# Kernel tuning notes

Measured on AMD Instinct MI355X. Metric: run time of the kernel, lower is better.

## Reference

```python
import jax, jax.numpy as jnp
import numpy as np

B, T, C = 2, 2048, 1024
H = 16
HD = C // H  # head_size = 64
FF = 2 * C   # ffwd_size default = n_embd * 2
EPS = float(jnp.finfo(jnp.float32).eps)  # torch RMSNorm eps=None -> finfo eps


def rmsnorm(x, g):
    # torch.nn.RMSNorm: x / sqrt(mean(x^2) + eps) * weight
    ms = jnp.mean(jnp.square(x), axis=-1, keepdims=True)
    return x * jax.lax.rsqrt(ms + EPS) * g


def setup_inputs() -> dict:
    key = jax.random.key(0)
    ks = jax.random.split(key, 12)
    s_in = 1.0 / np.sqrt(C)
    s_ff = 1.0 / np.sqrt(FF)
    return {
        "target": jax.random.normal(ks[0], (B, T, C), dtype=jnp.float32),
        # per-head projections, torch Linear layout [out, in] stacked over heads: [H, HD, C]
        "wq": jax.random.uniform(ks[1], (H, HD, C), jnp.float32, -s_in, s_in),
        "wk": jax.random.uniform(ks[2], (H, HD, C), jnp.float32, -s_in, s_in),
        "wv": jax.random.uniform(ks[3], (H, HD, C), jnp.float32, -s_in, s_in),
        "w_proj": jax.random.uniform(ks[4], (C, H * HD), jnp.float32, -s_in, s_in),
        "b_proj": jax.random.uniform(ks[5], (C,), jnp.float32, -s_in, s_in),
        "w1": jax.random.uniform(ks[6], (FF, C), jnp.float32, -s_in, s_in),
        "b1": jax.random.uniform(ks[7], (FF,), jnp.float32, -s_in, s_in),
        "w2": jax.random.uniform(ks[8], (C, FF), jnp.float32, -s_ff, s_ff),
        "b2": jax.random.uniform(ks[9], (C,), jnp.float32, -s_ff, s_ff),
        "g1": jnp.ones((C,), jnp.float32),
        "g2": jnp.ones((C,), jnp.float32),
    }


def reference(target, wq, wk, wv, w_proj, b_proj, w1, b1, w2, b2, g1, g2):
    x = rmsnorm(target, g1)
    # q,k,v: [B,H,T,HD]
    q = jnp.einsum("btc,hdc->bhtd", x, wq)
    k = jnp.einsum("btc,hdc->bhtd", x, wk)
    v = jnp.einsum("btc,hdc->bhtd", x, wv)
    scale = HD ** -0.5
    wei = jnp.einsum("bhtd,bhsd->bhts", q, k) * scale  # [B,H,T,T]
    causal = jnp.tril(jnp.ones((T, T), dtype=bool))
    wei = jnp.where(causal, wei, -jnp.inf)
    wei = jax.nn.softmax(wei, axis=-1)
    attn = jnp.einsum("bhts,bhsd->bhtd", wei, v)  # [B,H,T,HD]
    attn = attn.transpose(0, 2, 1, 3).reshape(B, T, H * HD)  # concat heads
    attn = attn @ w_proj.T + b_proj
    target = target + attn
    y = rmsnorm(target, g2)
    h = jax.nn.gelu(y @ w1.T + b1, approximate=False)  # torch nn.GELU default = exact
    ff = h @ w2.T + b2
    return target + ff
```

## Files before the change

### kernel.cpp

```cpp
#include <hip/hip_runtime.h>
#include <math.h>

#define B_  2
#define T_  2048
#define C_  1024
#define H_  16
#define HD_ 64
#define FF_ 2048
#define EPS_ 1.1920929e-07f

typedef __attribute__((ext_vector_type(8))) short short8;
typedef __attribute__((ext_vector_type(4))) float f32x4;

__device__ __forceinline__ unsigned short f2bf(float f) {
    unsigned u = __float_as_uint(f);
    u += 0x7fffu + ((u >> 16) & 1u);
    return (unsigned short)(u >> 16);
}
__device__ __forceinline__ float bf2f(unsigned short u) {
    return __uint_as_float(((unsigned)u) << 16);
}

__global__ void prep_kernel(const float* __restrict__ wq, const float* __restrict__ wk,
                            const float* __restrict__ wv, const float* __restrict__ wp,
                            const float* __restrict__ w1, const float* __restrict__ w2,
                            unsigned short* __restrict__ wb,
                            const float* __restrict__ x, const float* __restrict__ g,
                            unsigned short* __restrict__ y) {
    int tid = threadIdx.x;
    if (blockIdx.x < 8192) {
        size_t i = ((size_t)blockIdx.x * 256 + tid) * 4;
        const float* src; size_t off = i;
        if      (i < 1048576u)  { src = wq; }
        else if (i < 2097152u)  { src = wk; off = i - 1048576u; }
        else if (i < 3145728u)  { src = wv; off = i - 2097152u; }
        else if (i < 4194304u)  { src = wp; off = i - 3145728u; }
        else if (i < 6291456u)  { src = w1; off = i - 4194304u; }
        else                    { src = w2; off = i - 6291456u; }
        float4 v4 = *(const float4*)(src + off);
        ushort4 o4;
        o4.x = f2bf(v4.x); o4.y = f2bf(v4.y); o4.z = f2bf(v4.z); o4.w = f2bf(v4.w);
        *(ushort4*)(wb + i) = o4;
    } else {
        int row = blockIdx.x - 8192;
        const float4* xr = (const float4*)(x + (size_t)row * C_);
        float4 xv = xr[tid];
        float ss = xv.x * xv.x + xv.y * xv.y + xv.z * xv.z + xv.w * xv.w;
        #pragma unroll
        for (int m = 32; m >= 1; m >>= 1) ss += __shfl_xor(ss, m, 64);
        __shared__ float sred[4];
        if ((tid & 63) == 0) sred[tid >> 6] = ss;
        __syncthreads();
        float tot = sred[0] + sred[1] + sred[2] + sred[3];
        float r = rsqrtf(tot * (1.0f / C_) + EPS_);
        float4 gv = ((const float4*)g)[tid];
        ushort4 o;
        o.x = f2bf(xv.x * r * gv.x);
        o.y = f2bf(xv.y * r * gv.y);
        o.z = f2bf(xv.z * r * gv.z);
        o.w = f2bf(xv.w * r * gv.w);
        *((ushort4*)(y + (size_t)row * C_) + tid) = o;
    }
}

__global__ void rmsnorm_bf16_kernel(const float* __restrict__ x, const float* __restrict__ g,
                                    unsigned short* __restrict__ y) {
    int row = blockIdx.x;
    int tid = threadIdx.x;
    const float4* xr = (const float4*)(x + (size_t)row * C_);
    float4 xv = xr[tid];
    float ss = xv.x * xv.x + xv.y * xv.y + xv.z * xv.z + xv.w * xv.w;
    #pragma unroll
    for (int m = 32; m >= 1; m >>= 1) ss += __shfl_xor(ss, m, 64);
    __shared__ float sred[4];
    if ((tid & 63) == 0) sred[tid >> 6] = ss;
    __syncthreads();
    float tot = sred[0] + sred[1] + sred[2] + sred[3];
    float r = rsqrtf(tot * (1.0f / C_) + EPS_);
    float4 gv = ((const float4*)g)[tid];
    ushort4 o;
    o.x = f2bf(xv.x * r * gv.x);
    o.y = f2bf(xv.y * r * gv.y);
    o.z = f2bf(xv.z * r * gv.z);
    o.w = f2bf(xv.w * r * gv.w);
    *((ushort4*)(y + (size_t)row * C_) + tid) = o;
}

template <int TM, int ACT, bool BIAS, bool RES, bool OBF16, int ROUTE>
__global__ __launch_bounds__(256) void mfma_gemm(
        const unsigned short* __restrict__ A, const unsigned short* __restrict__ W,
        const float* __restrict__ bias, const float* __restrict__ resid,
        void* __restrict__ O0, void* __restrict__ O1, void* __restrict__ O2,
        int M, int N, int K) {
    constexpr int ACH = TM / 8;
    constexpr int NCH = (ACH + 16) / 4;
    constexpr int MI  = TM / 32;
    __shared__ short As[2 * TM * 32];
    __shared__ short Bs[2 * 128 * 32];
    const int tid  = threadIdx.x;
    const int w    = tid >> 6, lane = tid & 63;
    const int tileN = blockIdx.x * 128, tileM = blockIdx.y * TM;

    const unsigned short* gsrc[NCH];
    short* ldst[NCH];
    #pragma unroll
    for (int i2 = 0; i2 < NCH; ++i2) {
        int c = w * NCH + i2;
        if (c < ACH) {
            int kh = c / (ACH / 2), lc = c % (ACH / 2);
            gsrc[i2] = A + (size_t)(tileM + lc * 16 + (lane >> 2)) * K + kh * 32 + (lane & 3) * 8;
            ldst[i2] = As + c * 512;
        } else {
            int c2 = c - ACH;
            int kh = c2 >> 3, lc = c2 & 7;
            gsrc[i2] = W + (size_t)(tileN + lc * 16 + (lane >> 2)) * K + kh * 32 + (lane & 3) * 8;
            ldst[i2] = Bs + c2 * 512;
        }
    }

    f32x4 acc[MI][4];
    const f32x4 zed = {0.f, 0.f, 0.f, 0.f};
    #pragma unroll
    for (int i = 0; i < MI; ++i)
        #pragma unroll
        for (int j = 0; j < 4; ++j) acc[i][j] = zed;

    const int wm = (w >> 1) * (TM / 2), wn = (w & 1) * 64;
    const int frow = lane & 15, koff = (lane >> 4) * 8;

    for (int k0 = 0; k0 < K; k0 += 64) {
        #pragma unroll
        for (int i2 = 0; i2 < NCH; ++i2)
            __builtin_amdgcn_global_load_lds(
                (const __attribute__((address_space(1))) unsigned*)(gsrc[i2] + k0),
                (__attribute__((address_space(3))) unsigned*)ldst[i2], 16, 0, 0);
        __syncthreads();

        #pragma unroll
        for (int kh = 0; kh < 2; ++kh) {
            short8 af[MI], bfr[4];
            #pragma unroll
            for (int i = 0; i < MI; ++i)
                af[i] = *(const short8*)(As + kh * TM * 32 + (wm + i * 16 + frow) * 32 + koff);
            #pragma unroll
            for (int j = 0; j < 4; ++j)
                bfr[j] = *(const short8*)(Bs + kh * 128 * 32 + (wn + j * 16 + frow) * 32 + koff);
            #pragma unroll
            for (int i = 0; i < MI; ++i)
                #pragma unroll
                for (int j = 0; j < 4; ++j)
                    acc[i][j] = __builtin_amdgcn_mfma_f32_16x16x32_bf16(af[i], bfr[j], acc[i][j], 0, 0, 0);
        }
        __syncthreads();
    }

    const int ecol = lane & 15, erow = (lane >> 4) * 4;
    const int zone = ROUTE ? (tileN >> 10) : 0;
    #pragma unroll
    for (int j = 0; j < 4; ++j) {
        int n = tileN + wn + j * 16 + ecol;
        float bv = BIAS ? bias[n] : 0.f;
        int nl = ROUTE ? (n & 1023) : n;
        #pragma unroll
        for (int i = 0; i < MI; ++i) {
            int mbase = tileM + wm + i * 16 + erow;
            #pragma unroll
            for (int r = 0; r < 4; ++r) {
                float val = acc[i][j][r] + bv;
                if (ACT == 1) val = 0.5f * val * (1.0f + erff(val * 0.70710678118654752f));
                int mrow = mbase + r;
                if (ROUTE) {
                    if (zone == 0) {
                        ((unsigned short*)O0)[(size_t)mrow * 1024 + nl] = f2bf(val * 0.125f);
                    } else if (zone == 1) {
                        ((unsigned short*)O1)[(size_t)mrow * 1024 + nl] = f2bf(val);
                    } else {
                        int bb = mrow >> 11, tt = mrow & 2047;
                        int hh = nl >> 6, dd = nl & 63;
                        ((unsigned short*)O2)[((size_t)((bb * 16 + hh) * 64 + dd)) * 2048 + tt] = f2bf(val);
                    }
                } else {
                    size_t idx = (size_t)mrow * N + n;
                    if (RES) val += resid[idx];
                    if (OBF16) ((unsigned short*)O0)[idx] = f2bf(val);
                    else       ((float*)O0)[idx] = val;
                }
            }
        }
    }
}

__global__ __launch_bounds__(256) void flash_mfma_kernel(
        const unsigned short* __restrict__ q, const unsigned short* __restrict__ k,
        const unsigned short* __restrict__ vT, unsigned short* __restrict__ out) {
    __shared__ unsigned short Ks[64 * 72];
    __shared__ unsigned short Vt[64 * 72];
    __shared__ unsigned short Ps[2 * 4 * 16 * 40];

    const int tid  = threadIdx.x;
    const int w    = tid >> 6, lane = tid & 63;
    const int quad = lane >> 4, l15 = lane & 15;
    const int bh = blockIdx.x;
    const int qt = (gridDim.y - 1) - blockIdx.y;
    const int h = bh & (H_ - 1);
    const int b = bh >> 4;

    const size_t qkbase = (size_t)b * T_ * C_ + h * HD_;
    const size_t vbase  = (size_t)(b * H_ + h) * HD_ * T_;

    short8 QB[2];
    {
        const unsigned short* qp = q + qkbase + (size_t)(qt * 64 + w * 16 + l15) * C_;
        QB[0] = *(const short8*)(qp + quad * 8);
        QB[1] = *(const short8*)(qp + 32 + quad * 8);
    }

    f32x4 O[4];
    const f32x4 zed = {0.f, 0.f, 0.f, 0.f};
    #pragma unroll
    for (int dt = 0; dt < 4; ++dt) O[dt] = zed;
    float l_i = 0.f;

    const int qg = qt * 64 + w * 16 + l15;
    const int psoff = w * 640 + l15 * 40;
    const int sr = tid >> 3, sp = tid & 7;

    for (int st = 0; st <= qt; ++st) {
        const int s0 = st * 64;
        {
            const unsigned short* kp = k + qkbase + (size_t)(s0 + sr) * C_ + sp * 8;
            *(short8*)&Ks[sr * 72 + sp * 8]        = *(const short8*)kp;
            *(short8*)&Ks[(sr + 32) * 72 + sp * 8] = *(const short8*)(kp + 32 * C_);
            const unsigned short* vp = vT + vbase + (size_t)sr * T_ + s0 + sp * 8;
            *(short8*)&Vt[sr * 72 + sp * 8]        = *(const short8*)vp;
            *(short8*)&Vt[(sr + 32) * 72 + sp * 8] = *(const short8*)(vp + 32 * T_);
        }
        __syncthreads();

        const bool diag = (st == qt);
        #pragma unroll
        for (int sb = 0; sb < 2; ++sb) {
            const int sbl = sb * 32;
            f32x4 Sacc[2];
            #pragma unroll
            for (int u = 0; u < 2; ++u) {
                const unsigned short* kr = &Ks[(sbl + 16 * u + l15) * 72 + quad * 8];
                short8 KA0 = *(const short8*)kr;
                short8 KA1 = *(const short8*)(kr + 32);
                Sacc[u] = __builtin_amdgcn_mfma_f32_16x16x32_bf16(KA0, QB[0], zed, 0, 0, 0);
                Sacc[u] = __builtin_amdgcn_mfma_f32_16x16x32_bf16(KA1, QB[1], Sacc[u], 0, 0, 0);
            }
            float vals[8];
            if (diag) {
                #pragma unroll
                for (int u = 0; u < 2; ++u)
                    #pragma unroll
                    for (int r = 0; r < 4; ++r) {
                        int sg = s0 + sbl + 16 * u + quad * 4 + r;
                        vals[u * 4 + r] = (sg > qg) ? 0.f : __expf(Sacc[u][r]);
                    }
            } else {
                #pragma unroll
                for (int u = 0; u < 2; ++u)
                    #pragma unroll
                    for (int r = 0; r < 4; ++r)
                        vals[u * 4 + r] = __expf(Sacc[u][r]);
            }
            float rs = 0.f;
            #pragma unroll
            for (int i = 0; i < 8; ++i) rs += vals[i];
            rs += __shfl_xor(rs, 16, 64);
            rs += __shfl_xor(rs, 32, 64);
            l_i += rs;

            #pragma unroll
            for (int u = 0; u < 2; ++u) {
                uint2 pw;
                pw.x = (unsigned)f2bf(vals[u * 4 + 0]) | ((unsigned)f2bf(vals[u * 4 + 1]) << 16);
                pw.y = (unsigned)f2bf(vals[u * 4 + 2]) | ((unsigned)f2bf(vals[u * 4 + 3]) << 16);
                *(uint2*)&Ps[sb * 2560 + psoff + 16 * u + quad * 4] = pw;
            }
            __syncthreads();

            short8 PA = *(const short8*)&Ps[sb * 2560 + psoff + quad * 8];
            #pragma unroll
            for (int dt = 0; dt < 4; ++dt) {
                short8 VB = *(const short8*)&Vt[(16 * dt + l15) * 72 + sbl + quad * 8];
                O[dt] = __builtin_amdgcn_mfma_f32_16x16x32_bf16(PA, VB, O[dt], 0, 0, 0);
            }
        }
        __syncthreads();
    }

    f32x4 inv;
    #pragma unroll
    for (int r = 0; r < 4; ++r) inv[r] = 1.0f / __shfl(l_i, quad * 4 + r, 64);
    #pragma unroll
    for (int dt = 0; dt < 4; ++dt)
        #pragma unroll
        for (int r = 0; r < 4; ++r) {
            int row = qt * 64 + w * 16 + quad * 4 + r;
            int col = h * HD_ + dt * 16 + l15;
            out[((size_t)(b * T_ + row)) * C_ + col] = f2bf(O[dt][r] * inv[r]);
        }
}

extern "C" void kernel_launch(void* const* d_in, const int* in_sizes, int n_in,
                              void* d_out, int out_size, void* d_ws, size_t ws_size,
                              hipStream_t stream) {
    const float* target = (const float*)d_in[0];
    const float* wq     = (const float*)d_in[1];
    const float* wk     = (const float*)d_in[2];
    const float* wv     = (const float*)d_in[3];
    const float* w_proj = (const float*)d_in[4];
    const float* b_proj = (const float*)d_in[5];
    const float* w1     = (const float*)d_in[6];
    const float* b1     = (const float*)d_in[7];
    const float* w2     = (const float*)d_in[8];
    const float* b2     = (const float*)d_in[9];
    const float* g1     = (const float*)d_in[10];
    const float* g2     = (const float*)d_in[11];
    float* out = (float*)d_out;

    char* ws = (char*)d_ws;
    const size_t MB = 1u << 20;
    unsigned short* xn = (unsigned short*)(ws);
    unsigned short* q  = (unsigned short*)(ws + 8 * MB);
    unsigned short* k  = (unsigned short*)(ws + 16 * MB);
    unsigned short* vt = (unsigned short*)(ws + 24 * MB);
    float*          x2 = (float*)(ws + 32 * MB);
    unsigned short* wb = (unsigned short*)(ws + 48 * MB);
    unsigned short* y  = q;
    unsigned short* hb = k;

    unsigned short* wqkv_b = wb;
    unsigned short* wp_b   = wb + 3145728u;
    unsigned short* w1_b   = wb + 4194304u;
    unsigned short* w2_b   = wb + 6291456u;

    const int M = B_ * T_;

    prep_kernel<<<12288, 256, 0, stream>>>(wq, wk, wv, w_proj, w1, w2, wb, target, g1, xn);

    mfma_gemm<128, 0, false, false, true, 1><<<dim3(24, M / 128), 256, 0, stream>>>(
        xn, wqkv_b, nullptr, nullptr, q, k, vt, M, 3072, C_);

    flash_mfma_kernel<<<dim3(B_ * H_, T_ / 64), 256, 0, stream>>>(q, k, vt, xn);

    mfma_gemm<64, 0, true, true, false, 0><<<dim3(C_ / 128, M / 64), 256, 0, stream>>>(
        xn, wp_b, b_proj, target, x2, nullptr, nullptr, M, C_, C_);

    rmsnorm_bf16_kernel<<<M, 256, 0, stream>>>(x2, g2, y);

    mfma_gemm<64, 1, true, false, true, 0><<<dim3(FF_ / 128, M / 64), 256, 0, stream>>>(
        y, w1_b, b1, nullptr, hb, nullptr, nullptr, M, FF_, C_);

    mfma_gemm<64, 0, true, true, false, 0><<<dim3(C_ / 128, M / 64), 256, 0, stream>>>(
        hb, w2_b, b2, x2, out, nullptr, nullptr, M, C_, FF_);
}
```

Baseline: 288.3 us.

## Double-buffer K/V tiles via direct global-to-LDS loads with XOR swizzle in flash attention

The flash attention kernel now stages K and V tiles with global_load_lds into two alternating LDS buffers, so the next tile loads while the current one is computed. The padded LDS rows become an XOR-swizzled layout, presumably to avoid bank conflicts. The Q scale now folds in log2(e) so exp2 can replace expf, and the per-subblock barrier around the P write/read is replaced by a sched_barrier plus setprio around the MFMAs. Dropping that barrier is only safe if each wave reads back only its own P rows, and the swizzle must match between the staging and read sides.

```diff
diff --git a/kernel.cpp b/kernel.cpp
--- a/kernel.cpp
+++ b/kernel.cpp
@@ -171,7 +171,7 @@
                 int mrow = mbase + r;
                 if (ROUTE) {
                     if (zone == 0) {
-                        ((unsigned short*)O0)[(size_t)mrow * 1024 + nl] = f2bf(val * 0.125f);
+                        ((unsigned short*)O0)[(size_t)mrow * 1024 + nl] = f2bf(val * 0.18033688011112042f);
                     } else if (zone == 1) {
                         ((unsigned short*)O1)[(size_t)mrow * 1024 + nl] = f2bf(val);
                     } else {
@@ -193,8 +193,10 @@
 __global__ __launch_bounds__(256) void flash_mfma_kernel(
         const unsigned short* __restrict__ q, const unsigned short* __restrict__ k,
         const unsigned short* __restrict__ vT, unsigned short* __restrict__ out) {
-    __shared__ unsigned short Ks[64 * 72];
-    __shared__ unsigned short Vt[64 * 72];
+    __shared__ unsigned short KsA[64 * 64];
+    __shared__ unsigned short VtA[64 * 64];
+    __shared__ unsigned short KsB[64 * 64];
+    __shared__ unsigned short VtB[64 * 64];
     __shared__ unsigned short Ps[2 * 4 * 16 * 40];
 
     const int tid  = threadIdx.x;
@@ -223,30 +225,40 @@
 
     const int qg = qt * 64 + w * 16 + l15;
     const int psoff = w * 640 + l15 * 40;
-    const int sr = tid >> 3, sp = tid & 7;
-
-    for (int st = 0; st <= qt; ++st) {
-        const int s0 = st * 64;
-        {
-            const unsigned short* kp = k + qkbase + (size_t)(s0 + sr) * C_ + sp * 8;
-            *(short8*)&Ks[sr * 72 + sp * 8]        = *(const short8*)kp;
-            *(short8*)&Ks[(sr + 32) * 72 + sp * 8] = *(const short8*)(kp + 32 * C_);
-            const unsigned short* vp = vT + vbase + (size_t)sr * T_ + s0 + sp * 8;
-            *(short8*)&Vt[sr * 72 + sp * 8]        = *(const short8*)vp;
-            *(short8*)&Vt[(sr + 32) * 72 + sp * 8] = *(const short8*)(vp + 32 * T_);
-        }
-        __syncthreads();
-
-        const bool diag = (st == qt);
+    const int r8 = lane >> 3, c7 = lane & 7;
+    const int cswz = (c7 ^ r8) * 8;
+    const int swz15 = (l15 & 7);
+
+    auto stageKV = [&](unsigned short* Ksb, unsigned short* Vtb, int st_) {
+        const int s0_ = st_ * 64;
+        #pragma unroll
+        for (int c = 0; c < 2; ++c) {
+            const int row = w * 16 + c * 8 + r8;
+            const unsigned short* gk = k + qkbase + (size_t)(s0_ + row) * C_ + cswz;
+            __builtin_amdgcn_global_load_lds(
+                (const __attribute__((address_space(1))) unsigned*)gk,
+                (__attribute__((address_space(3))) unsigned*)(Ksb + (w * 16 + c * 8) * 64), 16, 0, 0);
+            const unsigned short* gv = vT + vbase + (size_t)row * T_ + s0_ + cswz;
+            __builtin_amdgcn_global_load_lds(
+                (const __attribute__((address_space(1))) unsigned*)gv,
+                (__attribute__((address_space(3))) unsigned*)(Vtb + (w * 16 + c * 8) * 64), 16, 0, 0);
+        }
+    };
+
+    auto computeTile = [&](const unsigned short* Ksb, const unsigned short* Vtb, int st_) {
+        const bool diag = (st_ == qt);
+        const int s0_ = st_ * 64;
         #pragma unroll
         for (int sb = 0; sb < 2; ++sb) {
             const int sbl = sb * 32;
             f32x4 Sacc[2];
             #pragma unroll
             for (int u = 0; u < 2; ++u) {
-                const unsigned short* kr = &Ks[(sbl + 16 * u + l15) * 72 + quad * 8];
-                short8 KA0 = *(const short8*)kr;
-                short8 KA1 = *(const short8*)(kr + 32);
+                const int row = sbl + 16 * u + l15;
+                const unsigned short* kr = Ksb + row * 64;
+                const int kc = (quad ^ swz15) * 8;
+                short8 KA0 = *(const short8*)(kr + kc);
+                short8 KA1 = *(const short8*)(kr + (kc ^ 32));
                 Sacc[u] = __builtin_amdgcn_mfma_f32_16x16x32_bf16(KA0, QB[0], zed, 0, 0, 0);
                 Sacc[u] = __builtin_amdgcn_mfma_f32_16x16x32_bf16(KA1, QB[1], Sacc[u], 0, 0, 0);
             }
@@ -256,15 +268,15 @@
                 for (int u = 0; u < 2; ++u)
                     #pragma unroll
                     for (int r = 0; r < 4; ++r) {
-                        int sg = s0 + sbl + 16 * u + quad * 4 + r;
-                        vals[u * 4 + r] = (sg > qg) ? 0.f : __expf(Sacc[u][r]);
+                        int sg = s0_ + sbl + 16 * u + quad * 4 + r;
+                        vals[u * 4 + r] = (sg > qg) ? 0.f : __builtin_amdgcn_exp2f(Sacc[u][r]);
                     }
             } else {
                 #pragma unroll
                 for (int u = 0; u < 2; ++u)
                     #pragma unroll
                     for (int r = 0; r < 4; ++r)
-                        vals[u * 4 + r] = __expf(Sacc[u][r]);
+                        vals[u * 4 + r] = __builtin_amdgcn_exp2f(Sacc[u][r]);
             }
             float rs = 0.f;
             #pragma unroll
@@ -280,16 +292,32 @@
                 pw.y = (unsigned)f2bf(vals[u * 4 + 2]) | ((unsigned)f2bf(vals[u * 4 + 3]) << 16);
                 *(uint2*)&Ps[sb * 2560 + psoff + 16 * u + quad * 4] = pw;
             }
-            __syncthreads();
+            __builtin_amdgcn_sched_barrier(0);
 
             short8 PA = *(const short8*)&Ps[sb * 2560 + psoff + quad * 8];
+            __builtin_amdgcn_s_setprio(1);
             #pragma unroll
             for (int dt = 0; dt < 4; ++dt) {
-                short8 VB = *(const short8*)&Vt[(16 * dt + l15) * 72 + sbl + quad * 8];
+                const int vrow = 16 * dt + l15;
+                short8 VB = *(const short8*)(Vtb + vrow * 64 + (((4 * sb + quad) ^ swz15) * 8));
                 O[dt] = __builtin_amdgcn_mfma_f32_16x16x32_bf16(PA, VB, O[dt], 0, 0, 0);
             }
-        }
-        __syncthreads();
+            __builtin_amdgcn_s_setprio(0);
+        }
+    };
+
+    stageKV(KsA, VtA, 0);
+    __syncthreads();
+    int st = 0;
+    for (;;) {
+        if (st + 1 <= qt) stageKV(KsB, VtB, st + 1);
+        computeTile(KsA, VtA, st);
+        __syncthreads();
+        ++st; if (st > qt) break;
+        if (st + 1 <= qt) stageKV(KsA, VtA, st + 1);
+        computeTile(KsB, VtB, st);
+        __syncthreads();
+        ++st; if (st > qt) break;
     }
 
     f32x4 inv;
```

Result: faster. 279.8 us (-3.0%).
